# Kernel optimization log

Measured on AMD Instinct MI355X. Metric: run time of the kernel, lower is better.

## Reference

```python
import jax, jax.numpy as jnp
import numpy as np

KS = 32          # kernel_size from __init__
EPS = 1e-10
CLAMP = 6.0


def _box_mean(a, ks):
    # stride-1 VALID average pool over the last two dims of an NCHW tensor
    s = jax.lax.reduce_window(a, 0.0, jax.lax.add,
                              window_dimensions=(1, 1, ks, ks),
                              window_strides=(1, 1, 1, 1),
                              padding='VALID')
    return s / float(ks * ks)


def _pad_reflect(a, pd):
    return jnp.pad(a, ((0, 0), (0, 0), (pd, pd), (pd, pd)), mode='reflect')


def setup_inputs() -> dict:
    key = jax.random.key(0)
    x = jax.random.normal(key, (32, 3, 512, 512), dtype=jnp.float32)
    return {"x": x}


def reference(x) -> jnp.ndarray:
    pd = KS // 2
    H, W = x.shape[-2], x.shape[-1]
    # local mean and mean-of-squares via reflect-padded box filters
    mean = _box_mean(_pad_reflect(x, pd), KS)[..., :H, :W]
    mean_sq = _box_mean(_pad_reflect(x * x, pd), KS)[..., :H, :W]
    std = jnp.sqrt(jnp.abs(mean_sq - mean * mean))
    return jnp.clip((x - mean) / (std + EPS), -CLAMP, CLAMP)
```

## Files before the change

### kernel.cpp

```cpp
#include <hip/hip_runtime.h>
#include <cstddef>
#include <cstdint>

#define H_    512
#define W_    512
#define NIMG  96
#define PD_   16
#define TY    64
#define NROWS (TY + 31)

template <int CTRL, int RMASK>
__device__ __forceinline__ float dpp_add(float x) {
    int t = __builtin_amdgcn_update_dpp(0, __float_as_int(x), CTRL, RMASK, 0xf, true);
    return x + __int_as_float(t);
}

__device__ __forceinline__ float wave_incl_scan(float x) {
    x = dpp_add<0x111, 0xf>(x);
    x = dpp_add<0x112, 0xf>(x);
    x = dpp_add<0x114, 0xf>(x);
    x = dpp_add<0x118, 0xf>(x);
    x = dpp_add<0x142, 0xa>(x);
    x = dpp_add<0x143, 0xc>(x);
    return x;
}

__device__ __forceinline__ float half_scan(float x) {
    x = dpp_add<0x111, 0xf>(x);
    x = dpp_add<0x112, 0xf>(x);
    x = dpp_add<0x114, 0xf>(x);
    x = dpp_add<0x118, 0xf>(x);
    x = dpp_add<0x142, 0xa>(x);
    return x;
}

__device__ __forceinline__ float bcast63(float x) {
    return __int_as_float(__builtin_amdgcn_readlane(__float_as_int(x), 63));
}
__device__ __forceinline__ float bperm(int addr, float v) {
    return __int_as_float(__builtin_amdgcn_ds_bpermute(addr, __float_as_int(v)));
}

__device__ __forceinline__ uint32_t cvt_pk_bf16(float a, float b) {
    uint32_t r;
    asm("v_cvt_pk_bf16_f32 %0, %1, %2" : "=v"(r) : "v"(a), "v"(b));
    return r;
}

__global__ void __launch_bounds__(128, 6)
localnorm_kernel(const float* __restrict__ xin, float* __restrict__ out)
{
    const int tid  = threadIdx.x;
    const int lane = tid & 63;
    const int wv   = tid >> 6;

    const int c0   = blockIdx.x * 128 + wv * 64;
    const int row0 = blockIdx.y * TY;
    const int img  = blockIdx.z;

    const float* __restrict__ src = xin + (size_t)img * (H_ * W_);
    float* __restrict__ dst = out + (size_t)img * (H_ * W_) + (size_t)row0 * W_ + c0 + lane;
    const float* __restrict__ xp = src + (size_t)row0 * W_ + c0 + lane;

    int pcm = c0 - PD_ + lane;
    const int ocm = (pcm < 0) ? -pcm : ((pcm > W_ - 1) ? 2 * (W_ - 1) - pcm : pcm);
    int pct = c0 - PD_ + 64 + (lane & 31);
    const int oct = (pct > W_ - 1) ? 2 * (W_ - 1) - pct : pct;
    const bool lo32 = lane < 32;

    const int A_dn  = ((lane + 31) & 63) << 2;
    const int A_u33 = ((lane - 33) & 63) << 2;
    const int A_u1  = ((lane - 1)  & 63) << 2;

    auto rowbase = [&](int p) {
        int r = row0 + p - PD_;
        r = (r < 0) ? -r : ((r > H_ - 1) ? 2 * (H_ - 1) - r : r);
        return src + (size_t)r * W_;
    };

    float gr[4], gtr[4];
#pragma unroll
    for (int p = 0; p < 4; ++p) {
        const float* rp = rowbase(p);
        gr[p]  = rp[ocm];
        gtr[p] = rp[oct];
    }

    uint32_t hist[32];
    float vmg = 0.f, vmq = 0.f, vt = 0.f;

#pragma unroll
    for (int p = 0; p < 31; ++p) {
        float g = gr[p & 3], gt = gtr[p & 3];
        {   const float* rp = rowbase(p + 4);
            gr[p & 3]  = rp[ocm];
            gtr[p & 3] = rp[oct];
        }
        uint32_t pk = cvt_pk_bf16(g, gt);
        hist[p] = pk;
        float fg  = __uint_as_float(pk << 16);
        float fgt = __uint_as_float(pk & 0xffff0000u);
        vmg += fg;
        vmq += fg * fg;
        vt  += lo32 ? fgt : fgt * fgt;
    }
    hist[31] = 0u;

    float xr[4];
#pragma unroll
    for (int k = 0; k < 4; ++k) xr[k] = xp[(size_t)k * W_];

    for (int pb = 0; pb < 2; ++pb) {
        const int ib = pb * 32;
#pragma unroll
        for (int k = 0; k < 32; ++k) {
            const int i = ib + k;
            float g = gr[(k + 3) & 3], gt = gtr[(k + 3) & 3];
            {   int pn = i + 35; if (pn > NROWS - 1) pn = NROWS - 1;
                const float* rp = rowbase(pn);
                gr[(k + 3) & 3]  = rp[ocm];
                gtr[(k + 3) & 3] = rp[oct];
            }
            float xv = xr[k & 3];
            {   int xn = i + 4; if (xn > TY - 1) xn = TY - 1;
                xr[k & 3] = xp[(size_t)xn * W_];
            }

            uint32_t pk  = cvt_pk_bf16(g, gt);
            uint32_t old = hist[(k + 31) & 31];
            hist[(k + 31) & 31] = pk;
            float fg  = __uint_as_float(pk << 16);
            float fgt = __uint_as_float(pk & 0xffff0000u);
            float og  = __uint_as_float(old << 16);
            float ogt = __uint_as_float(old & 0xffff0000u);
            vmg += fg - og;
            vmq += fg * fg;
            vmq -= og * og;
            float dtl = fgt - ogt;
            float dth = fgt * fgt - ogt * ogt;
            vt += lo32 ? dtl : dth;

            float sag = wave_incl_scan(vmg);
            float saq = wave_incl_scan(vmq);
            float sbt = half_scan(vt);
            float sa63g = bcast63(sag), sa63q = bcast63(saq);
            float dng = bperm(A_dn, sag);
            float dnq = bperm(A_dn, saq);
            float ubg = bperm(A_u33, sbt);
            float ubq = bperm(A_u1,  sbt);
            float slog = sag - vmg, sloq = saq - vmq;
            float shig = (lane <= 32) ? dng : (sa63g + ubg);
            float shiq = (lane <= 32) ? dnq : (sa63q + ubq);
            float sg = shig - slog;
            float sq = shiq - sloq;

            float mg = sg * (1.f / 1024.f);
            float mq = sq * (1.f / 1024.f);
            float sd = sqrtf(fabsf(mq - mg * mg)) + 1e-10f;
            float r  = __fdividef(xv - mg, sd);
            r = fminf(fmaxf(r, -6.f), 6.f);
            dst[(size_t)i * W_] = r;
        }
    }
}

extern "C" void kernel_launch(void* const* d_in, const int* in_sizes, int n_in,
                              void* d_out, int out_size, void* d_ws, size_t ws_size,
                              hipStream_t stream) {
    (void)in_sizes; (void)n_in; (void)d_ws; (void)ws_size; (void)out_size;
    const float* x = (const float*)d_in[0];
    float* o = (float*)d_out;
    dim3 grid(W_ / 128, H_ / TY, NIMG);
    localnorm_kernel<<<grid, dim3(128), 0, stream>>>(x, o);
}
```

Baseline: 215.7 us.

## Software-pipeline row scans with output stage and use rsq instead of sqrt+div

Splits each row's work into a front stage (loads, sliding-window update, DPP scans, cross-lane permutes) and a back stage (combine, normalize, store), interleaving row k's front with row k-1's back. The goal is to hide the ds_bpermute and readlane latency behind independent work. It also replaces sqrt plus fast divide with a single reciprocal square root using a tiny epsilon inside, which changes numerics slightly. The launch-bounds occupancy hint of 6 is dropped, and the fully unrolled 64-row loop with a two-entry pending struct may raise register pressure.

```diff
diff --git a/kernel.cpp b/kernel.cpp
--- a/kernel.cpp
+++ b/kernel.cpp
@@ -47,7 +47,15 @@
     return r;
 }
 
-__global__ void __launch_bounds__(128, 6)
+struct Pend {
+    float dng, dnq;
+    float ubg, ubq;
+    float s63g, s63q;
+    float slog, sloq;
+    float xv;
+};
+
+__global__ void __launch_bounds__(128)
 localnorm_kernel(const float* __restrict__ xin, float* __restrict__ out)
 {
     const int tid  = threadIdx.x;
@@ -110,58 +118,67 @@
 #pragma unroll
     for (int k = 0; k < 4; ++k) xr[k] = xp[(size_t)k * W_];
 
-    for (int pb = 0; pb < 2; ++pb) {
-        const int ib = pb * 32;
+    Pend P[2];
+
+    auto front = [&](int k, Pend& Q) {
+        float g = gr[(k + 3) & 3], gt = gtr[(k + 3) & 3];
+        {   int pn = k + 35; if (pn > NROWS - 1) pn = NROWS - 1;
+            const float* rp = rowbase(pn);
+            gr[(k + 3) & 3]  = rp[ocm];
+            gtr[(k + 3) & 3] = rp[oct];
+        }
+        Q.xv = xr[k & 3];
+        {   int xn = k + 4; if (xn > TY - 1) xn = TY - 1;
+            xr[k & 3] = xp[(size_t)xn * W_];
+        }
+
+        uint32_t pk  = cvt_pk_bf16(g, gt);
+        uint32_t old = hist[(k + 31) & 31];
+        hist[(k + 31) & 31] = pk;
+        float fg  = __uint_as_float(pk << 16);
+        float fgt = __uint_as_float(pk & 0xffff0000u);
+        float og  = __uint_as_float(old << 16);
+        float ogt = __uint_as_float(old & 0xffff0000u);
+        vmg += fg - og;
+        vmq += fg * fg;
+        vmq -= og * og;
+        float dtl = fgt - ogt;
+        float dth = fgt * fgt - ogt * ogt;
+        vt += lo32 ? dtl : dth;
+
+        float sag = wave_incl_scan(vmg);
+        float saq = wave_incl_scan(vmq);
+        float sbt = half_scan(vt);
+        Q.s63g = bcast63(sag);
+        Q.s63q = bcast63(saq);
+        Q.dng  = bperm(A_dn, sag);
+        Q.dnq  = bperm(A_dn, saq);
+        Q.ubg  = bperm(A_u33, sbt);
+        Q.ubq  = bperm(A_u1,  sbt);
+        Q.slog = sag - vmg;
+        Q.sloq = saq - vmq;
+    };
+
+    auto back = [&](int j, const Pend& Q) {
+        float shig = (lane <= 32) ? Q.dng : (Q.s63g + Q.ubg);
+        float shiq = (lane <= 32) ? Q.dnq : (Q.s63q + Q.ubq);
+        float sg = shig - Q.slog;
+        float sq = shiq - Q.sloq;
+        float mg = sg * (1.f / 1024.f);
+        float mq = sq * (1.f / 1024.f);
+        float var = fabsf(mq - mg * mg);
+        float r = (Q.xv - mg) * __builtin_amdgcn_rsqf(var + 1e-20f);
+        r = fminf(fmaxf(r, -6.f), 6.f);
+        dst[(size_t)j * W_] = r;
+    };
+
+    front(0, P[0]);
 #pragma unroll
-        for (int k = 0; k < 32; ++k) {
-            const int i = ib + k;
-            float g = gr[(k + 3) & 3], gt = gtr[(k + 3) & 3];
-            {   int pn = i + 35; if (pn > NROWS - 1) pn = NROWS - 1;
-                const float* rp = rowbase(pn);
-                gr[(k + 3) & 3]  = rp[ocm];
-                gtr[(k + 3) & 3] = rp[oct];
-            }
-            float xv = xr[k & 3];
-            {   int xn = i + 4; if (xn > TY - 1) xn = TY - 1;
-                xr[k & 3] = xp[(size_t)xn * W_];
-            }
-
-            uint32_t pk  = cvt_pk_bf16(g, gt);
-            uint32_t old = hist[(k + 31) & 31];
-            hist[(k + 31) & 31] = pk;
-            float fg  = __uint_as_float(pk << 16);
-            float fgt = __uint_as_float(pk & 0xffff0000u);
-            float og  = __uint_as_float(old << 16);
-            float ogt = __uint_as_float(old & 0xffff0000u);
-            vmg += fg - og;
-            vmq += fg * fg;
-            vmq -= og * og;
-            float dtl = fgt - ogt;
-            float dth = fgt * fgt - ogt * ogt;
-            vt += lo32 ? dtl : dth;
-
-            float sag = wave_incl_scan(vmg);
-            float saq = wave_incl_scan(vmq);
-            float sbt = half_scan(vt);
-            float sa63g = bcast63(sag), sa63q = bcast63(saq);
-            float dng = bperm(A_dn, sag);
-            float dnq = bperm(A_dn, saq);
-            float ubg = bperm(A_u33, sbt);
-            float ubq = bperm(A_u1,  sbt);
-            float slog = sag - vmg, sloq = saq - vmq;
-            float shig = (lane <= 32) ? dng : (sa63g + ubg);
-            float shiq = (lane <= 32) ? dnq : (sa63q + ubq);
-            float sg = shig - slog;
-            float sq = shiq - sloq;
-
-            float mg = sg * (1.f / 1024.f);
-            float mq = sq * (1.f / 1024.f);
-            float sd = sqrtf(fabsf(mq - mg * mg)) + 1e-10f;
-            float r  = __fdividef(xv - mg, sd);
-            r = fminf(fmaxf(r, -6.f), 6.f);
-            dst[(size_t)i * W_] = r;
-        }
+    for (int k = 1; k < TY; ++k) {
+        front(k, P[k & 1]);
+        back(k - 1, P[(k - 1) & 1]);
     }
+    back(TY - 1, P[(TY - 1) & 1]);
 }
 
 extern "C" void kernel_launch(void* const* d_in, const int* in_sizes, int n_in,
```

After: 246.2 us. 14.1% more time.
